# Performance work log

Measured on AMD Instinct MI355X. Metric: run time of the kernel, lower is better.

## Reference

```python
import jax, jax.numpy as jnp
import numpy as np

jax.config.update("jax_enable_x64", True)

P = 2013265921          # NTT-friendly prime 15 * 2**27 + 1 (int64-safe proxy for BLS12-377 Fr)
GEN = 31                # generator of the multiplicative group of F_P
LOGN = 22
N = 1 << LOGN           # domain_size
C = 4                   # columns, as in the module docstring example


def _pow_table(base, n):
    """powers[k] = base**k mod P for k in [0, n), built by repeated doubling (vectorized)."""
    pw = np.ones(n, dtype=np.int64)
    cur = base % P
    step = 1
    while step < n:
        hi = min(2 * step, n)
        pw[step:hi] = (pw[:hi - step] * cur) % P
        cur = (cur * cur) % P
        step *= 2
    return pw


def setup_inputs() -> dict:
    key = jax.random.key(0)
    x = jax.random.randint(key, (N, C), 0, P, dtype=jnp.int64)
    omega = pow(GEN, (P - 1) // N, P)          # primitive N-th root of unity
    omega_inv = pow(omega, P - 2, P)           # its inverse (Fermat)
    twiddles = jnp.asarray(_pow_table(omega_inv, N // 2))  # omega_inv**k, k < N/2  (the 'Params' table)
    n_inv = jnp.asarray(pow(N, P - 2, P), dtype=jnp.int64)  # N^{-1} mod P
    return {"input": x, "twiddles": twiddles, "n_inv": n_inv}


def reference(input, twiddles, n_inv):
    """Inverse NTT over F_P, columns transformed independently. Output in natural order."""
    n, c = input.shape
    logn = n.bit_length() - 1
    # bit-reversal permutation indices (static; computed with numpy)
    idx = np.arange(n)
    rev = np.zeros(n, dtype=np.int64)
    for i in range(logn):
        rev = (rev << 1) | ((idx >> i) & 1)
    x = input[rev]
    # iterative Cooley-Tukey butterflies, logn stages
    for s in range(1, logn + 1):
        m = 1 << s
        half = m >> 1
        w = twiddles[:: n // m]                 # [half] = omega_inv**(j * n/m)
        xr = x.reshape(-1, m, c)                # [n/m, m, c]
        lo, hi = xr[:, :half], xr[:, half:]
        t = (w[None, :, None] * hi) % P         # modular twiddle multiply
        x = jnp.concatenate([(lo + t) % P, (lo - t) % P], axis=1).reshape(n, c)
    return (x * n_inv) % P                      # scale by N^{-1}
```

## Files before the change

### kernel.cpp

```cpp
#include <hip/hip_runtime.h>
#include <stdint.h>

static constexpr uint32_t P = 2013265921u;
static constexpr int      LOGM = 11;
static constexpr int      MSZ  = 1 << LOGM;
static constexpr int      NCOL = 4;

__host__ __device__ constexpr uint32_t neg_pinv32() {
    uint32_t x = 1u;
    for (int i = 0; i < 5; ++i) x *= 2u - P * x;
    return 0u - x;
}
static constexpr uint32_t NEG_PINV = neg_pinv32();
static constexpr uint32_t R1 = (uint32_t)(((uint64_t)1 << 32) % P);
static constexpr uint32_t R2 = (uint32_t)(((uint64_t)R1 * R1) % P);

__device__ __forceinline__ uint32_t mont_mul(uint32_t a, uint32_t b) {
    uint32_t tlo = a * b;
    uint32_t thi = __umulhi(a, b);
    uint32_t m   = tlo * NEG_PINV;
    uint32_t r   = thi + __umulhi(m, P) + (tlo != 0u);
    uint32_t s   = r - P;
    return s < r ? s : r;
}
__device__ __forceinline__ uint32_t to_mont(uint32_t a) { return mont_mul(a, R2); }

__device__ __forceinline__ uint32_t shoup_mul(uint32_t w, uint32_t wp, uint32_t x) {
    uint32_t q = __umulhi(wp, x);
    uint32_t t = w * x - q * P;
    uint32_t s = t - P;
    return s < t ? s : t;
}
__device__ __forceinline__ uint32_t add_p(uint32_t a, uint32_t b) {
    uint32_t r = a + b, s = r - P; return s < r ? s : r;
}
__device__ __forceinline__ uint32_t sub_p(uint32_t a, uint32_t b) {
    uint32_t r = a - b, s = r + P; return s < r ? s : r;
}
__device__ __forceinline__ uint4 mm4(uint32_t w, uint4 v) {
    return make_uint4(mont_mul(w, v.x), mont_mul(w, v.y),
                      mont_mul(w, v.z), mont_mul(w, v.w));
}
__device__ __forceinline__ void bf4_sh(uint4& L, uint4& H, uint2 w) {
    uint4 t = make_uint4(shoup_mul(w.x, w.y, H.x), shoup_mul(w.x, w.y, H.y),
                         shoup_mul(w.x, w.y, H.z), shoup_mul(w.x, w.y, H.w));
    uint4 l = L;
    L = make_uint4(add_p(l.x, t.x), add_p(l.y, t.y), add_p(l.z, t.z), add_p(l.w, t.w));
    H = make_uint4(sub_p(l.x, t.x), sub_p(l.y, t.y), sub_p(l.z, t.z), sub_p(l.w, t.w));
}
__device__ __forceinline__ void bf4_mont(uint4& L, uint4& H, uint32_t wm) {
    uint4 t = mm4(wm, H);
    uint4 l = L;
    L = make_uint4(add_p(l.x, t.x), add_p(l.y, t.y), add_p(l.z, t.z), add_p(l.w, t.w));
    H = make_uint4(sub_p(l.x, t.x), sub_p(l.y, t.y), sub_p(l.z, t.z), sub_p(l.w, t.w));
}
__device__ __forceinline__ void bf4_triv(uint4& L, uint4& H) {
    uint4 l = L, h = H;
    L = make_uint4(add_p(l.x, h.x), add_p(l.y, h.y), add_p(l.z, h.z), add_p(l.w, h.w));
    H = make_uint4(sub_p(l.x, h.x), sub_p(l.y, h.y), sub_p(l.z, h.z), sub_p(l.w, h.w));
}

__device__ __forceinline__ int g_sw(int el) {
    return el ^ (((el >> 3) ^ (el >> 6)) & 7);
}
__device__ __forceinline__ int fidx(int el, int c4) { return (g_sw(el) << 2) | c4; }

__device__ __forceinline__ void radix8_sh(uint4 x[8],
        uint2 ta, uint2 tb0, uint2 tb1,
        uint2 tc0, uint2 tc1, uint2 tc2, uint2 tc3) {
    bf4_sh(x[0], x[1], ta);  bf4_sh(x[2], x[3], ta);
    bf4_sh(x[4], x[5], ta);  bf4_sh(x[6], x[7], ta);
    bf4_sh(x[0], x[2], tb0); bf4_sh(x[1], x[3], tb1);
    bf4_sh(x[4], x[6], tb0); bf4_sh(x[5], x[7], tb1);
    bf4_sh(x[0], x[4], tc0); bf4_sh(x[1], x[5], tc1);
    bf4_sh(x[2], x[6], tc2); bf4_sh(x[3], x[7], tc3);
}

template <bool PASS2>
__global__ __launch_bounds__(1024, 2) void intt_pass(
        const uint4* __restrict__ src, uint4* __restrict__ dst,
        const uint32_t* __restrict__ tw,
        const uint32_t* __restrict__ ninv_p)
{
    __shared__ uint4 buf[MSZ * NCOL];
    __shared__ uint2 stab[2048];

    const int      t   = threadIdx.x;
    const int      c4  = t & 3;
    const int      sub = t >> 2;
    const uint32_t bid = blockIdx.x;
    const uint32_t grp = ((bid & 7u) << 6) | (bid >> 3);
    const uint32_t c   = (grp << 2) | (uint32_t)c4;

    uint32_t wv[2]; int ev[2];
#pragma unroll
    for (int q = 0; q < 2; ++q) {
        int e = t + (q << 10);
        ev[q] = e;
        if (e < 2047) {
            uint32_t ep1 = (uint32_t)e + 1u;
            int sm1 = 31 - __clz((int)ep1);
            uint32_t j = ep1 - (1u << sm1);
            wv[q] = tw[j << (21 - sm1)];
        }
    }

    const uint32_t r8 = __brev((uint32_t)sub) >> 24;
    uint4 x[8];
#pragma unroll
    for (int m = 0; m < 8; ++m) {
        uint32_t r3 = __brev((uint32_t)m) >> 29;
        x[m] = src[((r3 << 8) | r8) * (uint32_t)MSZ + c];
    }

#pragma unroll
    for (int q = 0; q < 2; ++q) {
        if (ev[q] < 2047) {
            uint32_t w  = wv[q];
            uint32_t wp = (uint32_t)((((uint64_t)w) << 32) / P);
            stab[ev[q]] = make_uint2(w, wp);
        }
    }

    const uint32_t u1 = to_mont(tw[1u << 20]);
    const uint32_t u2 = to_mont(tw[1u << 19]);
    const uint32_t u3 = to_mont(tw[3u << 19]);

    bf4_triv(x[0], x[1]);  bf4_triv(x[2], x[3]);
    bf4_triv(x[4], x[5]);  bf4_triv(x[6], x[7]);
    bf4_triv(x[0], x[2]);  bf4_mont(x[1], x[3], u1);
    bf4_triv(x[4], x[6]);  bf4_mont(x[5], x[7], u1);
    bf4_triv(x[0], x[4]);  bf4_mont(x[1], x[5], u2);
    bf4_mont(x[2], x[6], u1); bf4_mont(x[3], x[7], u3);
#pragma unroll
    for (int m = 0; m < 8; ++m) buf[fidx(8 * sub + m, c4)] = x[m];
    __syncthreads();

    {
        const int L = sub & 7, hi = sub >> 3;
        const int base = (hi << 6) | L;
#pragma unroll
        for (int m = 0; m < 8; ++m) x[m] = buf[fidx(base | (m << 3), c4)];
        radix8_sh(x, stab[7 + L], stab[15 + L], stab[23 + L],
                     stab[31 + L], stab[39 + L], stab[47 + L], stab[55 + L]);
#pragma unroll
        for (int m = 0; m < 8; ++m) buf[fidx(base | (m << 3), c4)] = x[m];
    }
    __syncthreads();

    {
        const int L = sub & 63, hi = sub >> 6;
        const int base = (hi << 9) | L;
#pragma unroll
        for (int m = 0; m < 8; ++m) x[m] = buf[fidx(base | (m << 6), c4)];
        radix8_sh(x, stab[63 + L], stab[127 + L], stab[191 + L],
                     stab[255 + L], stab[319 + L], stab[383 + L], stab[447 + L]);
#pragma unroll
        for (int m = 0; m < 8; ++m) buf[fidx(base | (m << 6), c4)] = x[m];
    }
    __syncthreads();

    uint32_t nm = 0u, s256 = 0u, step512 = 0u, tm0 = 0u;
    if (PASS2) {
        nm = to_mont(*ninv_p);
    } else {
        s256    = to_mont(tw[c << 8]);
        step512 = mont_mul(s256, s256);
        tm0     = to_mont(tw[c * (uint32_t)sub]);
    }
#pragma unroll
    for (int gg = 0; gg < 2; ++gg) {
        const int lo = sub + (gg << 8);
        uint4 y[4];
#pragma unroll
        for (int m = 0; m < 4; ++m) y[m] = buf[fidx(lo | (m << 9), c4)];
        const uint2 t10  = stab[511 + lo];
        const uint2 t110 = stab[1023 + lo];
        const uint2 t111 = stab[1535 + lo];
        bf4_sh(y[0], y[1], t10);  bf4_sh(y[2], y[3], t10);
        bf4_sh(y[0], y[2], t110); bf4_sh(y[1], y[3], t111);

        if (!PASS2) {
            uint32_t tm = tm0;
#pragma unroll
            for (int m = 0; m < 4; ++m) {
                dst[c * (uint32_t)MSZ + (uint32_t)((m << 9) | lo)] = mm4(tm, y[m]);
                tm = mont_mul(tm, step512);
            }
            tm0 = mont_mul(tm0, s256);
        } else {
#pragma unroll
            for (int m = 0; m < 4; ++m)
                dst[(uint32_t)((m << 9) | lo) * (uint32_t)MSZ + c] = mm4(nm, y[m]);
        }
    }
}

extern "C" void kernel_launch(void* const* d_in, const int* in_sizes, int n_in,
                              void* d_out, int out_size, void* d_ws, size_t ws_size,
                              hipStream_t stream)
{
    const uint4*    x    = (const uint4*)d_in[0];
    const uint32_t* tw   = (const uint32_t*)d_in[1];
    const uint32_t* ninv = (const uint32_t*)d_in[2];
    uint4*          out  = (uint4*)d_out;

    intt_pass<false><<<dim3(512), dim3(1024), 0, stream>>>(x, out, tw, ninv);
    intt_pass<true ><<<dim3(512), dim3(1024), 0, stream>>>(out, out, tw, ninv);
}
```

Baseline: 201.2 us.

## Map one column per 256-thread block with half-size shared buffer exchange

Each block now handles a single 2048-point column with 256 threads instead of four columns with 1024 threads. The block exchanges data through a 1024-entry shared buffer in two halves gated by wavefront group, and recomputes the last-stage twiddles with Montgomery multiplies instead of reading them from a larger shared table. The aim is lower shared memory and register use per block, so more blocks fit per CU and latency is better hidden. The cost is many extra barriers, more serialized shared-memory exchange rounds, and 16-byte loads and stores that now come from four separate columns per block instead of contiguous ones.

Result: slower. 209.0 us (+3.9%).

```diff
diff --git a/kernel.cpp b/kernel.cpp
--- a/kernel.cpp
+++ b/kernel.cpp
@@ -4,7 +4,6 @@
 static constexpr uint32_t P = 2013265921u;
 static constexpr int      LOGM = 11;
 static constexpr int      MSZ  = 1 << LOGM;
-static constexpr int      NCOL = 4;
 
 __host__ __device__ constexpr uint32_t neg_pinv32() {
     uint32_t x = 1u;
@@ -60,10 +59,9 @@
     H = make_uint4(sub_p(l.x, h.x), sub_p(l.y, h.y), sub_p(l.z, h.z), sub_p(l.w, h.w));
 }
 
-__device__ __forceinline__ int g_sw(int el) {
-    return el ^ (((el >> 3) ^ (el >> 6)) & 7);
-}
-__device__ __forceinline__ int fidx(int el, int c4) { return (g_sw(el) << 2) | c4; }
+__device__ __forceinline__ int g_sw(int i) {
+    return i ^ (((i >> 3) ^ (i >> 6)) & 7);
+}
 
 __device__ __forceinline__ void radix8_sh(uint4 x[8],
         uint2 ta, uint2 tb0, uint2 tb1,
@@ -77,49 +75,38 @@
 }
 
 template <bool PASS2>
-__global__ __launch_bounds__(1024, 2) void intt_pass(
+__global__ __launch_bounds__(256, 7) void intt_pass(
         const uint4* __restrict__ src, uint4* __restrict__ dst,
         const uint32_t* __restrict__ tw,
         const uint32_t* __restrict__ ninv_p)
 {
-    __shared__ uint4 buf[MSZ * NCOL];
-    __shared__ uint2 stab[2048];
+    __shared__ uint4 buf[1024];
+    __shared__ uint2 stab[511];
 
     const int      t   = threadIdx.x;
-    const int      c4  = t & 3;
-    const int      sub = t >> 2;
+    const int      wp  = t >> 7;
     const uint32_t bid = blockIdx.x;
-    const uint32_t grp = ((bid & 7u) << 6) | (bid >> 3);
-    const uint32_t c   = (grp << 2) | (uint32_t)c4;
-
-    uint32_t wv[2]; int ev[2];
+    const uint32_t c   = ((bid & 7u) << 8) | (bid >> 3);
+
 #pragma unroll
     for (int q = 0; q < 2; ++q) {
-        int e = t + (q << 10);
-        ev[q] = e;
-        if (e < 2047) {
+        int e = t + (q << 8);
+        if (e < 511) {
             uint32_t ep1 = (uint32_t)e + 1u;
             int sm1 = 31 - __clz((int)ep1);
             uint32_t j = ep1 - (1u << sm1);
-            wv[q] = tw[j << (21 - sm1)];
+            uint32_t w = tw[j << (21 - sm1)];
+            uint32_t wps = (uint32_t)((((uint64_t)w) << 32) / P);
+            stab[e] = make_uint2(w, wps);
         }
     }
 
-    const uint32_t r8 = __brev((uint32_t)sub) >> 24;
+    const uint32_t r8 = __brev((uint32_t)t) >> 24;
     uint4 x[8];
 #pragma unroll
     for (int m = 0; m < 8; ++m) {
         uint32_t r3 = __brev((uint32_t)m) >> 29;
         x[m] = src[((r3 << 8) | r8) * (uint32_t)MSZ + c];
-    }
-
-#pragma unroll
-    for (int q = 0; q < 2; ++q) {
-        if (ev[q] < 2047) {
-            uint32_t w  = wv[q];
-            uint32_t wp = (uint32_t)((((uint64_t)w) << 32) / P);
-            stab[ev[q]] = make_uint2(w, wp);
-        }
     }
 
     const uint32_t u1 = to_mont(tw[1u << 20]);
@@ -132,33 +119,61 @@
     bf4_triv(x[4], x[6]);  bf4_mont(x[5], x[7], u1);
     bf4_triv(x[0], x[4]);  bf4_mont(x[1], x[5], u2);
     bf4_mont(x[2], x[6], u1); bf4_mont(x[3], x[7], u3);
-#pragma unroll
-    for (int m = 0; m < 8; ++m) buf[fidx(8 * sub + m, c4)] = x[m];
-    __syncthreads();
-
-    {
-        const int L = sub & 7, hi = sub >> 3;
-        const int base = (hi << 6) | L;
-#pragma unroll
-        for (int m = 0; m < 8; ++m) x[m] = buf[fidx(base | (m << 3), c4)];
-        radix8_sh(x, stab[7 + L], stab[15 + L], stab[23 + L],
-                     stab[31 + L], stab[39 + L], stab[47 + L], stab[55 + L]);
-#pragma unroll
-        for (int m = 0; m < 8; ++m) buf[fidx(base | (m << 3), c4)] = x[m];
-    }
-    __syncthreads();
-
-    {
-        const int L = sub & 63, hi = sub >> 6;
-        const int base = (hi << 9) | L;
-#pragma unroll
-        for (int m = 0; m < 8; ++m) x[m] = buf[fidx(base | (m << 6), c4)];
-        radix8_sh(x, stab[63 + L], stab[127 + L], stab[191 + L],
-                     stab[255 + L], stab[319 + L], stab[383 + L], stab[447 + L]);
-#pragma unroll
-        for (int m = 0; m < 8; ++m) buf[fidx(base | (m << 6), c4)] = x[m];
-    }
-    __syncthreads();
+
+    const int L1 = t & 7;
+    const int b1i = (((t >> 3) << 6) | L1) & 1023;
+    if (wp == 0) {
+#pragma unroll
+        for (int m = 0; m < 8; ++m) buf[g_sw((8 * t + m) & 1023)] = x[m];
+    }
+    __syncthreads();
+    if (wp == 0) {
+#pragma unroll
+        for (int m = 0; m < 8; ++m) x[m] = buf[g_sw(b1i | (m << 3))];
+    }
+    __syncthreads();
+    if (wp == 1) {
+#pragma unroll
+        for (int m = 0; m < 8; ++m) buf[g_sw((8 * t + m) & 1023)] = x[m];
+    }
+    __syncthreads();
+    if (wp == 1) {
+#pragma unroll
+        for (int m = 0; m < 8; ++m) x[m] = buf[g_sw(b1i | (m << 3))];
+    }
+    __syncthreads();
+
+    radix8_sh(x, stab[7 + L1], stab[15 + L1], stab[23 + L1],
+                 stab[31 + L1], stab[39 + L1], stab[47 + L1], stab[55 + L1]);
+
+    const int L2 = t & 63;
+    const int b2i = ((((t >> 6) & 1) << 9) | L2);
+    if (wp == 0) {
+#pragma unroll
+        for (int m = 0; m < 8; ++m) buf[g_sw(b1i | (m << 3))] = x[m];
+    }
+    __syncthreads();
+    if (wp == 0) {
+#pragma unroll
+        for (int m = 0; m < 8; ++m) x[m] = buf[g_sw(b2i | (m << 6))];
+    }
+    __syncthreads();
+    if (wp == 1) {
+#pragma unroll
+        for (int m = 0; m < 8; ++m) buf[g_sw(b1i | (m << 3))] = x[m];
+    }
+    __syncthreads();
+    if (wp == 1) {
+#pragma unroll
+        for (int m = 0; m < 8; ++m) x[m] = buf[g_sw(b2i | (m << 6))];
+    }
+    __syncthreads();
+
+    radix8_sh(x, stab[63 + L2], stab[127 + L2], stab[191 + L2],
+                 stab[255 + L2], stab[319 + L2], stab[383 + L2], stab[447 + L2]);
+
+    const uint32_t b0m = to_mont(tw[(uint32_t)t << 11]);
+    const uint32_t b1m = mont_mul(b0m, u2);
 
     uint32_t nm = 0u, s256 = 0u, step512 = 0u, tm0 = 0u;
     if (PASS2) {
@@ -166,32 +181,57 @@
     } else {
         s256    = to_mont(tw[c << 8]);
         step512 = mont_mul(s256, s256);
-        tm0     = to_mont(tw[c * (uint32_t)sub]);
-    }
+        tm0     = to_mont(tw[c * (uint32_t)t]);
+    }
+
+    __syncthreads();
+    if (wp == 0) {
+#pragma unroll
+        for (int m = 0; m < 8; ++m) buf[g_sw(b2i | (m << 6))] = x[m];
+    }
+    __syncthreads();
+    uint4 y0[2], y1[2], y2[2], y3[2];
 #pragma unroll
     for (int gg = 0; gg < 2; ++gg) {
-        const int lo = sub + (gg << 8);
-        uint4 y[4];
-#pragma unroll
-        for (int m = 0; m < 4; ++m) y[m] = buf[fidx(lo | (m << 9), c4)];
-        const uint2 t10  = stab[511 + lo];
-        const uint2 t110 = stab[1023 + lo];
-        const uint2 t111 = stab[1535 + lo];
-        bf4_sh(y[0], y[1], t10);  bf4_sh(y[2], y[3], t10);
-        bf4_sh(y[0], y[2], t110); bf4_sh(y[1], y[3], t111);
+        const int lo = (gg << 8) | t;
+        y0[gg] = buf[g_sw(lo)];
+        y1[gg] = buf[g_sw(512 | lo)];
+        const uint32_t bg  = gg ? b1m : b0m;
+        const uint32_t t10 = mont_mul(bg, bg);
+        bf4_mont(y0[gg], y1[gg], t10);
+    }
+    __syncthreads();
+    if (wp == 1) {
+#pragma unroll
+        for (int m = 0; m < 8; ++m) buf[g_sw(b2i | (m << 6))] = x[m];
+    }
+    __syncthreads();
+#pragma unroll
+    for (int gg = 0; gg < 2; ++gg) {
+        const int lo = (gg << 8) | t;
+        y2[gg] = buf[g_sw(lo)];
+        y3[gg] = buf[g_sw(512 | lo)];
+        const uint32_t bg   = gg ? b1m : b0m;
+        const uint32_t t10  = mont_mul(bg, bg);
+        const uint32_t t111 = mont_mul(bg, u1);
+        bf4_mont(y2[gg], y3[gg], t10);
+        bf4_mont(y0[gg], y2[gg], bg);
+        bf4_mont(y1[gg], y3[gg], t111);
 
         if (!PASS2) {
-            uint32_t tm = tm0;
-#pragma unroll
-            for (int m = 0; m < 4; ++m) {
-                dst[c * (uint32_t)MSZ + (uint32_t)((m << 9) | lo)] = mm4(tm, y[m]);
-                tm = mont_mul(tm, step512);
-            }
-            tm0 = mont_mul(tm0, s256);
+            uint32_t tm = gg ? mont_mul(tm0, s256) : tm0;
+            dst[c * (uint32_t)MSZ + (uint32_t)lo]          = mm4(tm, y0[gg]);
+            tm = mont_mul(tm, step512);
+            dst[c * (uint32_t)MSZ + (uint32_t)(512 | lo)]  = mm4(tm, y1[gg]);
+            tm = mont_mul(tm, step512);
+            dst[c * (uint32_t)MSZ + (uint32_t)(1024 | lo)] = mm4(tm, y2[gg]);
+            tm = mont_mul(tm, step512);
+            dst[c * (uint32_t)MSZ + (uint32_t)(1536 | lo)] = mm4(tm, y3[gg]);
         } else {
-#pragma unroll
-            for (int m = 0; m < 4; ++m)
-                dst[(uint32_t)((m << 9) | lo) * (uint32_t)MSZ + c] = mm4(nm, y[m]);
+            dst[(uint32_t)lo * (uint32_t)MSZ + c]          = mm4(nm, y0[gg]);
+            dst[(uint32_t)(512 | lo) * (uint32_t)MSZ + c]  = mm4(nm, y1[gg]);
+            dst[(uint32_t)(1024 | lo) * (uint32_t)MSZ + c] = mm4(nm, y2[gg]);
+            dst[(uint32_t)(1536 | lo) * (uint32_t)MSZ + c] = mm4(nm, y3[gg]);
         }
     }
 }
@@ -205,6 +245,6 @@
     const uint32_t* ninv = (const uint32_t*)d_in[2];
     uint4*          out  = (uint4*)d_out;
 
-    intt_pass<false><<<dim3(512), dim3(1024), 0, stream>>>(x, out, tw, ninv);
-    intt_pass<true ><<<dim3(512), dim3(1024), 0, stream>>>(out, out, tw, ninv);
-}
+    intt_pass<false><<<dim3(2048), dim3(256), 0, stream>>>(x, out, tw, ninv);
+    intt_pass<true ><<<dim3(2048), dim3(256), 0, stream>>>(out, out, tw, ninv);
+}
```
